# Kernel optimization log

Measured on AMD Instinct MI355X. Metric: run time of the kernel, lower is better.

Reference implementation:

```python
import jax, jax.numpy as jnp
import numpy as np

NUM_STEPS = 8
N_ETYPES = 4
N_GRAPHS = 64


def setup_inputs() -> dict:
    key = jax.random.key(0)
    ks = jax.random.split(key, 16)
    N, E, D = 50000, 500000, 128
    features = jax.random.normal(ks[0], (N, D), dtype=jnp.float32)
    src = jax.random.randint(ks[1], (E,), 0, N, dtype=jnp.int32)
    dst = jax.random.randint(ks[2], (E,), 0, N, dtype=jnp.int32)
    edge_types = jax.random.randint(ks[3], (E,), 0, N_ETYPES, dtype=jnp.int32)
    graph_ids = jnp.sort(jax.random.randint(ks[4], (N,), 0, N_GRAPHS, dtype=jnp.int32))
    s = 1.0 / np.sqrt(D)
    # per-edge-type Linear(out,out): W[t] has shape [out,in], applied as x @ W.T + b
    W_etype = jax.random.uniform(ks[5], (N_ETYPES, D, D), jnp.float32, -s, s)
    b_etype = jax.random.uniform(ks[6], (N_ETYPES, D), jnp.float32, -s, s)
    # torch GRUCell(D, D) params
    W_ih = jax.random.uniform(ks[7], (3 * D, D), jnp.float32, -s, s)
    W_hh = jax.random.uniform(ks[8], (3 * D, D), jnp.float32, -s, s)
    b_ih = jax.random.uniform(ks[9], (3 * D,), jnp.float32, -s, s)
    b_hh = jax.random.uniform(ks[10], (3 * D,), jnp.float32, -s, s)
    cls_w = jax.random.uniform(ks[11], (1, D), jnp.float32, -s, s)
    cls_b = jax.random.uniform(ks[12], (1,), jnp.float32, -s, s)
    return dict(features=features, src=src, dst=dst, edge_types=edge_types,
                graph_ids=graph_ids, W_etype=W_etype, b_etype=b_etype,
                W_ih=W_ih, W_hh=W_hh, b_ih=b_ih, b_hh=b_hh,
                cls_w=cls_w, cls_b=cls_b)


def reference(features, src, dst, edge_types, graph_ids,
              W_etype, b_etype, W_ih, W_hh, b_ih, b_hh, cls_w, cls_b):
    N = features.shape[0]

    def step(h, _):
        # transform every node's state under every edge-type linear: [T, N, D]
        T = jnp.einsum('nd,tod->tno', h, W_etype) + b_etype[:, None, :]
        msg = T[edge_types, src]                      # [E, D] gather per edge
        a = jax.ops.segment_sum(msg, dst, num_segments=N)  # scatter-sum to dst
        # torch GRUCell
        gi = a @ W_ih.T + b_ih
        gh = h @ W_hh.T + b_hh
        i_r, i_z, i_n = jnp.split(gi, 3, axis=-1)
        h_r, h_z, h_n = jnp.split(gh, 3, axis=-1)
        r = jax.nn.sigmoid(i_r + h_r)
        z = jax.nn.sigmoid(i_z + h_z)
        n = jnp.tanh(i_n + r * h_n)
        h_new = (1.0 - z) * n + z * h
        return h_new, None

    h, _ = jax.lax.scan(step, features, None, length=NUM_STEPS)
    graph_sum = jax.ops.segment_sum(h, graph_ids, num_segments=N_GRAPHS)  # [B, D]
    logits = graph_sum @ cls_w.T + cls_b                                   # [B, 1]
    return jax.nn.sigmoid(logits).squeeze(-1)                              # [B]
```

## Files before the change

kernel.cpp:

```cpp
#include <hip/hip_runtime.h>

typedef __attribute__((ext_vector_type(4))) float floatx4;
typedef __attribute__((ext_vector_type(8))) _Float16 half8;

union H2 { unsigned int u; _Float16 h[2]; };

__device__ __forceinline__ float hs2f(unsigned short u) {
    union { unsigned short u; _Float16 h; } c; c.u = u; return (float)c.h;
}
__device__ __forceinline__ unsigned short f2hs(float f) {
    union { unsigned short u; _Float16 h; } c; c.h = (_Float16)f; return c.u;
}
__device__ __forceinline__ unsigned int pack2h(float a, float b) {
    H2 c; c.h[0] = (_Float16)a; c.h[1] = (_Float16)b; return c.u;
}

__device__ __forceinline__ void load_lds16(const unsigned short* g, unsigned short* l) {
    __builtin_amdgcn_global_load_lds(
        (__attribute__((address_space(1))) void*)(g),
        (__attribute__((address_space(3))) void*)(l), 16, 0, 0);
}

__global__ void k_hist(const int* __restrict__ dst, const int* __restrict__ et,
                       int* __restrict__ cnt4, int E) {
    int i = blockIdx.x * 256 + threadIdx.x;
    if (i < E) {
        atomicAdd(&cnt4[dst[i] * 4 + et[i]], 1);
    }
}

__global__ void k_scan_blk(const int* __restrict__ cnt4, int* __restrict__ row_ptr,
                           int* __restrict__ bsum, int N) {
    __shared__ int sm[256];
    int b = blockIdx.x, t = threadIdx.x, i = b * 256 + t;
    int v = 0;
    if (i < N) {
        const int4 q = ((const int4*)cnt4)[i];
        v = q.x + q.y + q.z + q.w;
    }
    sm[t] = v;
    __syncthreads();
    for (int off = 1; off < 256; off <<= 1) {
        int x = (t >= off) ? sm[t - off] : 0;
        __syncthreads();
        sm[t] += x;
        __syncthreads();
    }
    if (i < N) row_ptr[i] = sm[t] - v;
    if (t == 255) bsum[b] = sm[255];
}

__global__ void k_scan_top(int* __restrict__ bsum, int* __restrict__ boff,
                           int* __restrict__ row_ptr, int nblocks, int N) {
    __shared__ int sm[256];
    int t = threadIdx.x;
    int v = (t < nblocks) ? bsum[t] : 0;
    sm[t] = v;
    __syncthreads();
    for (int off = 1; off < 256; off <<= 1) {
        int x = (t >= off) ? sm[t - off] : 0;
        __syncthreads();
        sm[t] += x;
        __syncthreads();
    }
    if (t < nblocks) boff[t] = sm[t] - v;
    if (t == 255) row_ptr[N] = sm[255];
}

__global__ void k_scan_add(int* __restrict__ row_ptr, int* __restrict__ cursor4,
                           const int* __restrict__ boff, const int* __restrict__ cnt4, int N) {
    int i = blockIdx.x * 256 + threadIdx.x;
    if (i < N) {
        int r = row_ptr[i] + boff[blockIdx.x];
        row_ptr[i] = r;
        const int4 q = ((const int4*)cnt4)[i];
        int4 c;
        c.x = r;
        c.y = r + q.x;
        c.z = r + q.x + q.y;
        c.w = r + q.x + q.y + q.z;
        ((int4*)cursor4)[i] = c;
    }
}

__global__ void k_scatter(const int* __restrict__ src, const int* __restrict__ dst,
                          const int* __restrict__ et, int* __restrict__ cursor4,
                          int* __restrict__ edge_pk, int E, int Nn) {
    int i = blockIdx.x * 256 + threadIdx.x;
    if (i < E) {
        int p = atomicAdd(&cursor4[dst[i] * 4 + et[i]], 1);
        edge_pk[p] = et[i] * Nn + src[i];
    }
}

__global__ void k_init_h(const float* __restrict__ feat, unsigned short* __restrict__ AH, int N) {
    int i = blockIdx.x * 256 + threadIdx.x;
    if (i < N * 128) {
        int v = i >> 7, d = i & 127;
        AH[(size_t)v * 256 + 128 + d] = f2hs(feat[i]);
    }
}

__global__ void k_prep_wc2(const float* __restrict__ W, unsigned short* __restrict__ w) {
    int i = blockIdx.x * 256 + threadIdx.x;
    if (i < 65536) w[i] = f2hs(W[i]);
}

__global__ void k_prep_wrz(const float* __restrict__ Wih, const float* __restrict__ Whh,
                           unsigned short* __restrict__ w) {
    int i = blockIdx.x * 256 + threadIdx.x;
    if (i < 256 * 256) {
        int j = i >> 8, k = i & 255;
        float v = (k < 128) ? Wih[j * 128 + k] : Whh[j * 128 + (k - 128)];
        w[i] = f2hs(v);
    }
}

__global__ void k_prep_wnh(const float* __restrict__ Wih, const float* __restrict__ Whh,
                           unsigned short* __restrict__ win, unsigned short* __restrict__ whn) {
    int i = blockIdx.x * 256 + threadIdx.x;
    if (i < 128 * 128) {
        int c = i >> 7, k = i & 127;
        win[i] = f2hs(Wih[(256 + c) * 128 + k]);
        whn[i] = f2hs(Whh[(256 + c) * 128 + k]);
    }
}

__global__ __launch_bounds__(256) void k_gemm_pre(
    const unsigned short* __restrict__ AH, int M, int Nn,
    const unsigned short* __restrict__ Wc2,
    unsigned short* __restrict__ T)
{
    __shared__ __align__(16) unsigned short As[2][64 * 32];
    __shared__ __align__(16) unsigned short Bs[2][128 * 32];
    const int tid  = threadIdx.x;
    const int lane = tid & 63;
    const int wv   = tid >> 6;
    const int wm   = (wv & 1) * 32;
    const int wn   = (wv >> 1) * 64;
    const int mBase = blockIdx.x * 64;
    const int y    = blockIdx.y;
    const int srow = tid >> 2;
    const int sseg = (tid & 3) * 8;
    const int Ktot = 128;
    const unsigned short* Bw = Wc2 + (size_t)y * 128 * 128;

    floatx4 acc[2][4];
#pragma unroll
    for (int i = 0; i < 2; ++i)
#pragma unroll
        for (int j = 0; j < 4; ++j) acc[i][j] = (floatx4){0.f, 0.f, 0.f, 0.f};

    int r0 = mBase + srow; if (r0 >= M) r0 = M - 1;

    for (int k0 = 0; k0 < Ktot; k0 += 64) {
        __syncthreads();
#pragma unroll
        for (int sub = 0; sub < 2; ++sub) {
            const int ko = k0 + sub * 32;
            load_lds16(AH + (size_t)r0 * 256 + 128 + ko + sseg, &As[sub][srow * 32 + sseg]);
            const unsigned short* bw = Bw + (size_t)srow * Ktot + ko + sseg;
            load_lds16(bw,                     &Bs[sub][srow * 32 + sseg]);
            load_lds16(bw + (size_t)64 * Ktot, &Bs[sub][(srow + 64) * 32 + sseg]);
        }
        __syncthreads();
        const int kof = (lane >> 4) * 8;
        const int mr  = lane & 15;
#pragma unroll
        for (int p = 0; p < 2; ++p) {
            half8 af[2], bf[4];
#pragma unroll
            for (int i = 0; i < 2; ++i) af[i] = *(const half8*)&As[p][(wm + i * 16 + mr) * 32 + kof];
#pragma unroll
            for (int j = 0; j < 4; ++j) bf[j] = *(const half8*)&Bs[p][(wn + j * 16 + mr) * 32 + kof];
#pragma unroll
            for (int i = 0; i < 2; ++i)
#pragma unroll
                for (int j = 0; j < 4; ++j)
                    acc[i][j] = __builtin_amdgcn_mfma_f32_16x16x32_f16(af[i], bf[j], acc[i][j], 0, 0, 0);
        }
    }

    const int mr4 = (lane >> 4) * 4;
    const int nc  = lane & 15;
#pragma unroll
    for (int i = 0; i < 2; ++i) {
#pragma unroll
        for (int r = 0; r < 4; ++r) {
            int row = mBase + wm + i * 16 + mr4 + r;
            if (row < M) {
#pragma unroll
                for (int j = 0; j < 4; ++j) {
                    int col = wn + j * 16 + nc;
                    T[((size_t)y * Nn + row) * 128 + col] = f2hs(acc[i][j][r]);
                }
            }
        }
    }
}

__global__ __launch_bounds__(256) void k_aggregate2(
    const int* __restrict__ row_ptr, const int* __restrict__ cnt4,
    const int* __restrict__ edge_pk,
    const unsigned short* __restrict__ T, const float* __restrict__ b_et,
    unsigned short* __restrict__ AH, int N)
{
    const int wv = threadIdx.x >> 6;
    const int lane = threadIdx.x & 63;
    const int v0 = blockIdx.x * 8 + wv * 2;
    if (v0 >= N) return;
    const int v1 = v0 + 1;
    const bool has1 = (v1 < N);

    const int beg0 = __builtin_amdgcn_readfirstlane(row_ptr[v0]);
    const int end0 = __builtin_amdgcn_readfirstlane(row_ptr[v0 + 1]);
    const int end1 = has1 ? __builtin_amdgcn_readfirstlane(row_ptr[v1 + 1]) : end0;

    float a0x = 0, a0y = 0, a1x = 0, a1y = 0;
    const unsigned short* tbase = T + lane * 2;

    for (int e = beg0; e < end1; e += 12) {
        int sp[12];
        unsigned int hv[12];
#pragma unroll
        for (int u = 0; u < 12; ++u) {
            int idx = e + u;
            if (idx > end1 - 1) idx = end1 - 1;
            sp[u] = edge_pk[idx];
        }
#pragma unroll
        for (int u = 0; u < 12; ++u)
            hv[u] = *(const unsigned int*)(tbase + (size_t)sp[u] * 128);
#pragma unroll
        for (int u = 0; u < 12; ++u) {
            const int idx = e + u;
            if (idx < end1) {
                H2 c; c.u = hv[u];
                float x0 = (float)c.h[0];
                float x1 = (float)c.h[1];
                if (idx < end0) { a0x += x0; a0y += x1; }
                else            { a1x += x0; a1y += x1; }
            }
        }
    }

    const float2 b0 = *(const float2*)&b_et[0 * 128 + lane * 2];
    const float2 b1 = *(const float2*)&b_et[1 * 128 + lane * 2];
    const float2 b2 = *(const float2*)&b_et[2 * 128 + lane * 2];
    const float2 b3 = *(const float2*)&b_et[3 * 128 + lane * 2];
    {
        const int4 q = ((const int4*)cnt4)[v0];
        float bx = (float)q.x * b0.x + (float)q.y * b1.x + (float)q.z * b2.x + (float)q.w * b3.x;
        float by = (float)q.x * b0.y + (float)q.y * b1.y + (float)q.z * b2.y + (float)q.w * b3.y;
        *(unsigned int*)&AH[(size_t)v0 * 256 + lane * 2] = pack2h(a0x + bx, a0y + by);
    }
    if (has1) {
        const int4 q = ((const int4*)cnt4)[v1];
        float bx = (float)q.x * b0.x + (float)q.y * b1.x + (float)q.z * b2.x + (float)q.w * b3.x;
        float by = (float)q.x * b0.y + (float)q.y * b1.y + (float)q.z * b2.y + (float)q.w * b3.y;
        *(unsigned int*)&AH[(size_t)v1 * 256 + lane * 2] = pack2h(a1x + bx, a1y + by);
    }
}

__global__ __launch_bounds__(256) void k_gemm1(
    const unsigned short* __restrict__ A, int M,
    const unsigned short* __restrict__ Wrz,
    const unsigned short* __restrict__ Win, const unsigned short* __restrict__ Whn,
    _Float16* __restrict__ G)
{
    __shared__ __align__(16) unsigned short As[2][64 * 32];
    __shared__ __align__(16) unsigned short Bs[2][128 * 32];
    const int tid  = threadIdx.x;
    const int lane = tid & 63;
    const int wv   = tid >> 6;
    const int wm   = (wv & 1) * 32;
    const int wn   = (wv >> 1) * 64;
    const int mBase = blockIdx.x * 64;
    const int y    = blockIdx.y;
    const int srow = tid >> 2;
    const int sseg = (tid & 3) * 8;

    const unsigned short* Bw;
    int Ktot, aOff, colBase;
    if (y < 2)      { Bw = Wrz + (size_t)y * 128 * 256; Ktot = 256; aOff = 0;   colBase = y * 128; }
    else if (y == 2){ Bw = Win; Ktot = 128; aOff = 0;   colBase = 256; }
    else            { Bw = Whn; Ktot = 128; aOff = 128; colBase = 384; }

    floatx4 acc[2][4];
#pragma unroll
    for (int i = 0; i < 2; ++i)
#pragma unroll
        for (int j = 0; j < 4; ++j) acc[i][j] = (floatx4){0.f, 0.f, 0.f, 0.f};

    int r0 = mBase + srow; if (r0 >= M) r0 = M - 1;

    for (int k0 = 0; k0 < Ktot; k0 += 64) {
        __syncthreads();
#pragma unroll
        for (int sub = 0; sub < 2; ++sub) {
            const int ko = k0 + sub * 32;
            load_lds16(A + (size_t)r0 * 256 + aOff + ko + sseg, &As[sub][srow * 32 + sseg]);
            const unsigned short* bw = Bw + (size_t)srow * Ktot + ko + sseg;
            load_lds16(bw,                     &Bs[sub][srow * 32 + sseg]);
            load_lds16(bw + (size_t)64 * Ktot, &Bs[sub][(srow + 64) * 32 + sseg]);
        }
        __syncthreads();
        const int kof = (lane >> 4) * 8;
        const int mr  = lane & 15;
#pragma unroll
        for (int p = 0; p < 2; ++p) {
            half8 af[2], bf[4];
#pragma unroll
            for (int i = 0; i < 2; ++i) af[i] = *(const half8*)&As[p][(wm + i * 16 + mr) * 32 + kof];
#pragma unroll
            for (int j = 0; j < 4; ++j) bf[j] = *(const half8*)&Bs[p][(wn + j * 16 + mr) * 32 + kof];
#pragma unroll
            for (int i = 0; i < 2; ++i)
#pragma unroll
                for (int j = 0; j < 4; ++j)
                    acc[i][j] = __builtin_amdgcn_mfma_f32_16x16x32_f16(af[i], bf[j], acc[i][j], 0, 0, 0);
        }
    }

    const int mr4 = (lane >> 4) * 4;
    const int nc  = lane & 15;
#pragma unroll
    for (int i = 0; i < 2; ++i) {
#pragma unroll
        for (int r = 0; r < 4; ++r) {
            int row = mBase + wm + i * 16 + mr4 + r;
            if (row < M) {
#pragma unroll
                for (int j = 0; j < 4; ++j) {
                    int col = colBase + wn + j * 16 + nc;
                    G[(size_t)row * 512 + col] = (_Float16)acc[i][j][r];
                }
            }
        }
    }
}

__global__ void k_gru(const _Float16* __restrict__ G, unsigned short* __restrict__ AH,
                      const float* __restrict__ b_ih, const float* __restrict__ b_hh, int N) {
    int i = blockIdx.x * 256 + threadIdx.x;
    if (i >= N * 64) return;
    int v = i >> 6, j = i & 63;
    const unsigned int* g32 = (const unsigned int*)(G + (size_t)v * 512);
    H2 pr, pz, pn, ph;
    pr.u = g32[j];
    pz.u = g32[64 + j];
    pn.u = g32[128 + j];
    ph.u = g32[192 + j];
    H2 hv; hv.u = *(const unsigned int*)&AH[(size_t)v * 256 + 128 + j * 2];
    float outs[2];
#pragma unroll
    for (int q = 0; q < 2; ++q) {
        int d = j * 2 + q;
        float pre_r = (float)pr.h[q] + b_ih[d]       + b_hh[d];
        float pre_z = (float)pz.h[q] + b_ih[128 + d] + b_hh[128 + d];
        float i_n   = (float)pn.h[q] + b_ih[256 + d];
        float h_n   = (float)ph.h[q] + b_hh[256 + d];
        float r = 1.f / (1.f + __expf(-pre_r));
        float z = 1.f / (1.f + __expf(-pre_z));
        float n = tanhf(i_n + r * h_n);
        float h = (float)hv.h[q];
        outs[q] = (1.f - z) * n + z * h;
    }
    *(unsigned int*)&AH[(size_t)v * 256 + 128 + j * 2] = pack2h(outs[0], outs[1]);
}

__global__ void k_dotv(const unsigned short* __restrict__ AH, const float* __restrict__ cls_w,
                       float* __restrict__ dotv, int N) {
    int v = blockIdx.x * 4 + (threadIdx.x >> 6);
    int lane = threadIdx.x & 63;
    if (v >= N) return;
    H2 c; c.u = *(const unsigned int*)&AH[(size_t)v * 256 + 128 + lane * 2];
    float x = (float)c.h[0] * cls_w[lane * 2]
            + (float)c.h[1] * cls_w[lane * 2 + 1];
#pragma unroll
    for (int off = 32; off > 0; off >>= 1) x += __shfl_down(x, off);
    if (lane == 0) dotv[v] = x;
}

__global__ void k_gsum(const float* __restrict__ dotv, const int* __restrict__ gids,
                       const float* __restrict__ cls_b, float* __restrict__ out, int N) {
    int g = blockIdx.x;
    int t = threadIdx.x;
    int lo = 0, hi = N;
    while (lo < hi) { int m = (lo + hi) >> 1; if (gids[m] < g) lo = m + 1; else hi = m; }
    int s = lo;
    lo = 0; hi = N;
    while (lo < hi) { int m = (lo + hi) >> 1; if (gids[m] < g + 1) lo = m + 1; else hi = m; }
    int e = lo;
    float acc = 0.f;
    for (int v = s + t; v < e; v += 256) acc += dotv[v];
    __shared__ float red[256];
    red[t] = acc;
    __syncthreads();
    for (int off = 128; off > 0; off >>= 1) {
        if (t < off) red[t] += red[t + off];
        __syncthreads();
    }
    if (t == 0) out[g] = 1.f / (1.f + expf(-(red[0] + cls_b[0])));
}

extern "C" void kernel_launch(void* const* d_in, const int* in_sizes, int n_in,
                              void* d_out, int out_size, void* d_ws, size_t ws_size,
                              hipStream_t stream) {
    const float* features = (const float*)d_in[0];
    const int*   src      = (const int*)d_in[1];
    const int*   dst      = (const int*)d_in[2];
    const int*   etype    = (const int*)d_in[3];
    const int*   gids     = (const int*)d_in[4];
    const float* W_etype  = (const float*)d_in[5];
    const float* b_etype  = (const float*)d_in[6];
    const float* W_ih     = (const float*)d_in[7];
    const float* W_hh     = (const float*)d_in[8];
    const float* b_ih     = (const float*)d_in[9];
    const float* b_hh     = (const float*)d_in[10];
    const float* cls_w    = (const float*)d_in[11];
    const float* cls_b    = (const float*)d_in[12];
    const int N = in_sizes[0] / 128;
    const int E = in_sizes[1];
    float* out = (float*)d_out;

    char* ws = (char*)d_ws;
    size_t off = 0;
    auto alloc = [&](size_t bytes) -> void* {
        off = (off + 255) & ~(size_t)255;
        void* p = ws + off;
        off += bytes;
        return p;
    };
    unsigned short* AH  = (unsigned short*)alloc((size_t)N * 256 * 2);
    unsigned short* T   = (unsigned short*)alloc((size_t)4 * N * 128 * 2);
    _Float16*       G   = (_Float16*)alloc((size_t)N * 512 * 2);
    unsigned short* Wc2 = (unsigned short*)alloc(4 * 128 * 128 * 2);
    unsigned short* Wrz = (unsigned short*)alloc(256 * 256 * 2);
    unsigned short* Win = (unsigned short*)alloc(128 * 128 * 2);
    unsigned short* Whn = (unsigned short*)alloc(128 * 128 * 2);
    int* row_ptr = (int*)alloc((size_t)(N + 1) * 4);
    int* cursor4 = (int*)alloc((size_t)N * 16);
    int* cnt4    = (int*)alloc((size_t)N * 16);
    int* edge_pk = (int*)alloc((size_t)E * 4);
    float* dotv  = (float*)alloc((size_t)N * 4);
    int* bsum    = (int*)alloc(256 * 4);
    int* boff    = (int*)alloc(256 * 4);
    (void)ws_size; (void)n_in;

    const int nscan = (N + 255) / 256;
    hipMemsetAsync(cnt4, 0, (size_t)N * 16, stream);
    k_hist<<<(E + 255) / 256, 256, 0, stream>>>(dst, etype, cnt4, E);
    k_scan_blk<<<nscan, 256, 0, stream>>>(cnt4, row_ptr, bsum, N);
    k_scan_top<<<1, 256, 0, stream>>>(bsum, boff, row_ptr, nscan, N);
    k_scan_add<<<nscan, 256, 0, stream>>>(row_ptr, cursor4, boff, cnt4, N);
    k_scatter<<<(E + 255) / 256, 256, 0, stream>>>(src, dst, etype, cursor4, edge_pk, E, N);
    k_init_h<<<(N * 128 + 255) / 256, 256, 0, stream>>>(features, AH, N);
    k_prep_wc2<<<65536 / 256, 256, 0, stream>>>(W_etype, Wc2);
    k_prep_wrz<<<(256 * 256) / 256, 256, 0, stream>>>(W_ih, W_hh, Wrz);
    k_prep_wnh<<<(128 * 128) / 256, 256, 0, stream>>>(W_ih, W_hh, Win, Whn);

    const int mblocks64 = (N + 63) / 64;
    for (int s = 0; s < 8; ++s) {
        dim3 gp(mblocks64, 4);
        k_gemm_pre<<<gp, 256, 0, stream>>>(AH, N, N, Wc2, T);
        k_aggregate2<<<(N + 7) / 8, 256, 0, stream>>>(row_ptr, cnt4, edge_pk, T, b_etype, AH, N);
        dim3 g2(mblocks64, 4);
        k_gemm1<<<g2, 256, 0, stream>>>(AH, N, Wrz, Win, Whn, G);
        k_gru<<<(N * 64 + 255) / 256, 256, 0, stream>>>(G, AH, b_ih, b_hh, N);
    }
    k_dotv<<<(N + 3) / 4, 256, 0, stream>>>(AH, cls_w, dotv, N);
    k_gsum<<<out_size, 256, 0, stream>>>(dotv, gids, cls_b, out, N);
}
```

Baseline: 942.5 us.

## Fuse GRU gate GEMM with elementwise GRU update using per-slab column tiling

The gate GEMM and the separate GRU elementwise kernel are merged into one kernel. Each block now computes a 32-column slab of all four gate outputs (r, z, i_n, h_n), so the sigmoid/tanh update can run in the epilogue. This removes the fp16 G intermediate write and read and one kernel launch per step. Ping-pong state buffers avoid read-after-write hazards on h. In exchange, A tiles are reloaded once per slab across 4 slabs, each block does less MFMA work per LDS load, and the epilogue's scalar 2-byte stores are uncoalesced.

```diff
diff --git a/kernel.cpp b/kernel.cpp
--- a/kernel.cpp
+++ b/kernel.cpp
@@ -262,111 +262,104 @@
     }
 }
 
-__global__ __launch_bounds__(256) void k_gemm1(
-    const unsigned short* __restrict__ A, int M,
-    const unsigned short* __restrict__ Wrz,
-    const unsigned short* __restrict__ Win, const unsigned short* __restrict__ Whn,
-    _Float16* __restrict__ G)
+__global__ __launch_bounds__(256) void k_gates1(
+    const unsigned short* __restrict__ AHc,
+    unsigned short* __restrict__ AHn,
+    int M,
+    const unsigned short* __restrict__ Wr,
+    const unsigned short* __restrict__ Wz,
+    const unsigned short* __restrict__ Wi,
+    const unsigned short* __restrict__ Wh,
+    const float* __restrict__ b_ih, const float* __restrict__ b_hh)
 {
     __shared__ __align__(16) unsigned short As[2][64 * 32];
-    __shared__ __align__(16) unsigned short Bs[2][128 * 32];
+    __shared__ __align__(16) unsigned short Bs[2][3][32 * 32];
     const int tid  = threadIdx.x;
     const int lane = tid & 63;
     const int wv   = tid >> 6;
     const int wm   = (wv & 1) * 32;
-    const int wn   = (wv >> 1) * 64;
+    const int wn   = (wv >> 1) * 16;
     const int mBase = blockIdx.x * 64;
-    const int y    = blockIdx.y;
+    const int slab = blockIdx.y;
     const int srow = tid >> 2;
     const int sseg = (tid & 3) * 8;
-
-    const unsigned short* Bw;
-    int Ktot, aOff, colBase;
-    if (y < 2)      { Bw = Wrz + (size_t)y * 128 * 256; Ktot = 256; aOff = 0;   colBase = y * 128; }
-    else if (y == 2){ Bw = Win; Ktot = 128; aOff = 0;   colBase = 256; }
-    else            { Bw = Whn; Ktot = 128; aOff = 128; colBase = 384; }
+    const int kof  = (lane >> 4) * 8;
+    const int mr   = lane & 15;
+
+    int r0 = mBase + srow; if (r0 >= M) r0 = M - 1;
 
     floatx4 acc[2][4];
 #pragma unroll
     for (int i = 0; i < 2; ++i)
 #pragma unroll
-        for (int j = 0; j < 4; ++j) acc[i][j] = (floatx4){0.f, 0.f, 0.f, 0.f};
-
-    int r0 = mBase + srow; if (r0 >= M) r0 = M - 1;
-
-    for (int k0 = 0; k0 < Ktot; k0 += 64) {
+        for (int g = 0; g < 4; ++g) acc[i][g] = (floatx4){0.f, 0.f, 0.f, 0.f};
+
+    const int t2   = tid & 127;
+    const int brow = slab * 32 + (t2 >> 2);
+    const int bseg = (t2 & 3) * 8;
+
+    for (int k0 = 0; k0 < 256; k0 += 64) {
+        const bool ahalf = (k0 < 128);
         __syncthreads();
 #pragma unroll
         for (int sub = 0; sub < 2; ++sub) {
-            const int ko = k0 + sub * 32;
-            load_lds16(A + (size_t)r0 * 256 + aOff + ko + sseg, &As[sub][srow * 32 + sseg]);
-            const unsigned short* bw = Bw + (size_t)srow * Ktot + ko + sseg;
-            load_lds16(bw,                     &Bs[sub][srow * 32 + sseg]);
-            load_lds16(bw + (size_t)64 * Ktot, &Bs[sub][(srow + 64) * 32 + sseg]);
-        }
-        __syncthreads();
-        const int kof = (lane >> 4) * 8;
-        const int mr  = lane & 15;
+            const int ks = k0 + sub * 32;
+            load_lds16(AHc + (size_t)r0 * 256 + ks + sseg, &As[sub][srow * 32 + sseg]);
+            const unsigned short* bsrc = (tid < 128)
+                ? Wr + (size_t)brow * 256 + ks + bseg
+                : Wz + (size_t)brow * 256 + ks + bseg;
+            load_lds16(bsrc, &Bs[sub][0][0] + tid * 8);
+            if (tid < 128) {
+                const unsigned short* b3 = ahalf
+                    ? Wi + (size_t)brow * 128 + ks + bseg
+                    : Wh + (size_t)brow * 128 + (ks - 128) + bseg;
+                load_lds16(b3, &Bs[sub][2][0] + tid * 8);
+            }
+        }
+        __syncthreads();
 #pragma unroll
         for (int p = 0; p < 2; ++p) {
-            half8 af[2], bf[4];
+            half8 af[2], br_, bz_, b3_;
 #pragma unroll
             for (int i = 0; i < 2; ++i) af[i] = *(const half8*)&As[p][(wm + i * 16 + mr) * 32 + kof];
-#pragma unroll
-            for (int j = 0; j < 4; ++j) bf[j] = *(const half8*)&Bs[p][(wn + j * 16 + mr) * 32 + kof];
-#pragma unroll
-            for (int i = 0; i < 2; ++i)
-#pragma unroll
-                for (int j = 0; j < 4; ++j)
-                    acc[i][j] = __builtin_amdgcn_mfma_f32_16x16x32_f16(af[i], bf[j], acc[i][j], 0, 0, 0);
+            br_ = *(const half8*)&Bs[p][0][(wn + mr) * 32 + kof];
+            bz_ = *(const half8*)&Bs[p][1][(wn + mr) * 32 + kof];
+            b3_ = *(const half8*)&Bs[p][2][(wn + mr) * 32 + kof];
+#pragma unroll
+            for (int i = 0; i < 2; ++i) {
+                acc[i][0] = __builtin_amdgcn_mfma_f32_16x16x32_f16(af[i], br_, acc[i][0], 0, 0, 0);
+                acc[i][1] = __builtin_amdgcn_mfma_f32_16x16x32_f16(af[i], bz_, acc[i][1], 0, 0, 0);
+                if (ahalf) acc[i][2] = __builtin_amdgcn_mfma_f32_16x16x32_f16(af[i], b3_, acc[i][2], 0, 0, 0);
+                else       acc[i][3] = __builtin_amdgcn_mfma_f32_16x16x32_f16(af[i], b3_, acc[i][3], 0, 0, 0);
+            }
         }
     }
 
     const int mr4 = (lane >> 4) * 4;
     const int nc  = lane & 15;
+    const int col = slab * 32 + wn + nc;
+    const float b_r  = b_ih[col]       + b_hh[col];
+    const float b_z  = b_ih[128 + col] + b_hh[128 + col];
+    const float b_in = b_ih[256 + col];
+    const float b_hn = b_hh[256 + col];
 #pragma unroll
     for (int i = 0; i < 2; ++i) {
 #pragma unroll
         for (int r = 0; r < 4; ++r) {
             int row = mBase + wm + i * 16 + mr4 + r;
             if (row < M) {
-#pragma unroll
-                for (int j = 0; j < 4; ++j) {
-                    int col = colBase + wn + j * 16 + nc;
-                    G[(size_t)row * 512 + col] = (_Float16)acc[i][j][r];
-                }
+                float rv = acc[i][0][r] + b_r;
+                float zv = acc[i][1][r] + b_z;
+                float iv = acc[i][2][r] + b_in;
+                float hv = acc[i][3][r] + b_hn;
+                rv = 1.f / (1.f + __expf(-rv));
+                zv = 1.f / (1.f + __expf(-zv));
+                float nv = tanhf(iv + rv * hv);
+                float h = hs2f(AHc[(size_t)row * 256 + 128 + col]);
+                AHn[(size_t)row * 256 + 128 + col] = f2hs((1.f - zv) * nv + zv * h);
             }
         }
     }
-}
-
-__global__ void k_gru(const _Float16* __restrict__ G, unsigned short* __restrict__ AH,
-                      const float* __restrict__ b_ih, const float* __restrict__ b_hh, int N) {
-    int i = blockIdx.x * 256 + threadIdx.x;
-    if (i >= N * 64) return;
-    int v = i >> 6, j = i & 63;
-    const unsigned int* g32 = (const unsigned int*)(G + (size_t)v * 512);
-    H2 pr, pz, pn, ph;
-    pr.u = g32[j];
-    pz.u = g32[64 + j];
-    pn.u = g32[128 + j];
-    ph.u = g32[192 + j];
-    H2 hv; hv.u = *(const unsigned int*)&AH[(size_t)v * 256 + 128 + j * 2];
-    float outs[2];
-#pragma unroll
-    for (int q = 0; q < 2; ++q) {
-        int d = j * 2 + q;
-        float pre_r = (float)pr.h[q] + b_ih[d]       + b_hh[d];
-        float pre_z = (float)pz.h[q] + b_ih[128 + d] + b_hh[128 + d];
-        float i_n   = (float)pn.h[q] + b_ih[256 + d];
-        float h_n   = (float)ph.h[q] + b_hh[256 + d];
-        float r = 1.f / (1.f + __expf(-pre_r));
-        float z = 1.f / (1.f + __expf(-pre_z));
-        float n = tanhf(i_n + r * h_n);
-        float h = (float)hv.h[q];
-        outs[q] = (1.f - z) * n + z * h;
-    }
-    *(unsigned int*)&AH[(size_t)v * 256 + 128 + j * 2] = pack2h(outs[0], outs[1]);
 }
 
 __global__ void k_dotv(const unsigned short* __restrict__ AH, const float* __restrict__ cls_w,
@@ -432,9 +425,9 @@
         off += bytes;
         return p;
     };
-    unsigned short* AH  = (unsigned short*)alloc((size_t)N * 256 * 2);
+    unsigned short* A0  = (unsigned short*)alloc((size_t)N * 256 * 2);
+    unsigned short* A1  = (unsigned short*)alloc((size_t)N * 256 * 2);
     unsigned short* T   = (unsigned short*)alloc((size_t)4 * N * 128 * 2);
-    _Float16*       G   = (_Float16*)alloc((size_t)N * 512 * 2);
     unsigned short* Wc2 = (unsigned short*)alloc(4 * 128 * 128 * 2);
     unsigned short* Wrz = (unsigned short*)alloc(256 * 256 * 2);
     unsigned short* Win = (unsigned short*)alloc(128 * 128 * 2);
@@ -455,20 +448,24 @@
     k_scan_top<<<1, 256, 0, stream>>>(bsum, boff, row_ptr, nscan, N);
     k_scan_add<<<nscan, 256, 0, stream>>>(row_ptr, cursor4, boff, cnt4, N);
     k_scatter<<<(E + 255) / 256, 256, 0, stream>>>(src, dst, etype, cursor4, edge_pk, E, N);
-    k_init_h<<<(N * 128 + 255) / 256, 256, 0, stream>>>(features, AH, N);
+    k_init_h<<<(N * 128 + 255) / 256, 256, 0, stream>>>(features, A0, N);
     k_prep_wc2<<<65536 / 256, 256, 0, stream>>>(W_etype, Wc2);
     k_prep_wrz<<<(256 * 256) / 256, 256, 0, stream>>>(W_ih, W_hh, Wrz);
     k_prep_wnh<<<(128 * 128) / 256, 256, 0, stream>>>(W_ih, W_hh, Win, Whn);
 
     const int mblocks64 = (N + 63) / 64;
+    unsigned short* cur = A0;
+    unsigned short* nxt = A1;
     for (int s = 0; s < 8; ++s) {
         dim3 gp(mblocks64, 4);
-        k_gemm_pre<<<gp, 256, 0, stream>>>(AH, N, N, Wc2, T);
-        k_aggregate2<<<(N + 7) / 8, 256, 0, stream>>>(row_ptr, cnt4, edge_pk, T, b_etype, AH, N);
-        dim3 g2(mblocks64, 4);
-        k_gemm1<<<g2, 256, 0, stream>>>(AH, N, Wrz, Win, Whn, G);
-        k_gru<<<(N * 64 + 255) / 256, 256, 0, stream>>>(G, AH, b_ih, b_hh, N);
-    }
-    k_dotv<<<(N + 3) / 4, 256, 0, stream>>>(AH, cls_w, dotv, N);
+        k_gemm_pre<<<gp, 256, 0, stream>>>(cur, N, N, Wc2, T);
+        k_aggregate2<<<(N + 7) / 8, 256, 0, stream>>>(row_ptr, cnt4, edge_pk, T, b_etype, cur, N);
+        dim3 gg(mblocks64, 4);
+        k_gates1<<<gg, 256, 0, stream>>>(cur, nxt, N,
+                                         Wrz, Wrz + (size_t)128 * 256,
+                                         Win, Whn, b_ih, b_hh);
+        unsigned short* tmp = cur; cur = nxt; nxt = tmp;
+    }
+    k_dotv<<<(N + 3) / 4, 256, 0, stream>>>(cur, cls_w, dotv, N);
     k_gsum<<<out_size, 256, 0, stream>>>(dotv, gids, cls_b, out, N);
 }
```

After: 815.7 us, median of 3. 13.5% less time.
